# Kernel optimization log

Hardware: AMD Instinct MI355X
Metric: run time of the kernel (lower is better)

Reference implementation:

```python
import jax, jax.numpy as jnp
import numpy as np
import math

B, C, H, W, T, NH, SS = 4, 64, 32, 32, 32, 8, 512


def _alibi_slopes(heads):
    def pow2(n):
        start = 2 ** (-2 ** (-(math.log2(n) - 3)))
        return [start * start ** i for i in range(n)]
    if math.log2(heads).is_integer():
        return pow2(heads)
    cp = 2 ** math.floor(math.log2(heads))
    return pow2(cp) + pow2(2 * cp)[0::2][: heads - cp]


def _style_conv(x, style, weight, lw, lb, noise_p, bias_p, noise):
    # x: (b,c,h,w,t); weight: (out,in,1,1,1) -> modulated 1x1x1 grouped conv
    s = style @ lw.T + lb                                   # (b, in)
    w = weight[None] * s[:, None, :, None, None, None]       # (b,out,in,1,1,1)
    sigma_inv = jax.lax.rsqrt(jnp.sum(w * w, axis=(2, 3, 4, 5), keepdims=True) + 1e-8)
    w = (w * sigma_inv)[:, :, :, 0, 0, 0]                    # (b,out,in)
    y = jnp.einsum('bchwt,boc->bohwt', x, w)
    y = y + noise_p * noise                                  # (out,1,1,1)*(b,1,h,w,t)
    return y + bias_p


def setup_inputs() -> dict:
    key = jax.random.key(0)
    ks = jax.random.split(key, 8)
    return {
        'x': jax.random.normal(ks[0], (B, C, H, W, T), jnp.float32),
        'style': jax.random.normal(ks[1], (B, SS), jnp.float32),
        'qkv_w': jax.random.normal(ks[2], (3 * C, C, 1, 1, 1), jnp.float32),
        'qkv_lw': jax.random.normal(ks[3], (C, SS), jnp.float32) * 0.02,
        'qkv_lb': jnp.zeros((C,), jnp.float32),
        'qkv_np': jnp.zeros((3 * C, 1, 1, 1), jnp.float32),
        'qkv_bp': jnp.zeros((3 * C, 1, 1, 1), jnp.float32),
        'qkv_noise': jax.random.normal(ks[4], (B, 1, H, W, T), jnp.float32),
        'proj_w': jax.random.normal(ks[5], (C, C, 1, 1, 1), jnp.float32),
        'proj_lw': jax.random.normal(ks[6], (C, SS), jnp.float32) * 0.02,
        'proj_lb': jnp.zeros((C,), jnp.float32),
        'proj_np': jnp.zeros((C, 1, 1, 1), jnp.float32),
        'proj_bp': jnp.zeros((C, 1, 1, 1), jnp.float32),
        'proj_noise': jax.random.normal(ks[7], (B, 1, H, W, T), jnp.float32),
    }


def reference(x, style, qkv_w, qkv_lw, qkv_lb, qkv_np, qkv_bp, qkv_noise,
              proj_w, proj_lw, proj_lb, proj_np, proj_bp, proj_noise):
    b, c, h, w, t = x.shape
    qkv = _style_conv(x, style, qkv_w, qkv_lw, qkv_lb, qkv_np, qkv_bp, qkv_noise)
    q, k, v = jnp.split(qkv, 3, axis=1)                      # each (b,c,h,w,t)

    def to_heads(z):
        z = z.reshape(b, c * h * w, t).transpose(0, 2, 1)    # (b,t,chw)
        return z.reshape(b, t, NH, (c * h * w) // NH).transpose(0, 2, 1, 3)
    q, k, v = to_heads(q), to_heads(k), to_heads(v)          # (b,nh,t,dh)
    dh = q.shape[-1]

    attn = jnp.einsum('bnid,bnjd->bnij', q, k) / math.sqrt(dh)
    slopes = jnp.asarray(_alibi_slopes(NH), dtype=attn.dtype)[:, None, None]
    pos = -jnp.abs(jnp.arange(t)[None, :] - jnp.arange(t)[:, None]).astype(attn.dtype)
    attn = attn + slopes * pos                                # ALiBi bias
    # Faithful to original: masked_fill where tril(ones) is True (lower triangle masked)
    mask = jnp.tril(jnp.ones((t, t), bool))
    attn = jnp.where(mask, jnp.asarray(-1e18, attn.dtype), attn)
    attn = jax.nn.softmax(attn, axis=-1)
    out = jnp.einsum('bnij,bnjd->bnid', attn, v)              # (b,nh,t,dh)

    out = out.transpose(0, 2, 1, 3).reshape(b, t, c * h * w)  # (b,t,chw)
    out = out.reshape(b, t, c, h, w).transpose(0, 2, 3, 4, 1) # (b,c,h,w,t)
    return _style_conv(out, style, proj_w, proj_lw, proj_lb, proj_np, proj_bp, proj_noise)
```

## Files before the change

kernel.cpp:

```cpp
#include <hip/hip_runtime.h>

typedef unsigned short u16;
typedef unsigned int   u32;
typedef __attribute__((ext_vector_type(8))) short bf16x8;
typedef __attribute__((ext_vector_type(4))) float f32x4;

#define PP 32768
#define CC 64

__device__ __forceinline__ u16 f2b(float f) {
    u32 u; __builtin_memcpy(&u, &f, 4);
    u32 r = (u + 0x7FFFu + ((u >> 16) & 1u)) >> 16;
    return (u16)r;
}
__device__ __forceinline__ u32 pack2(float lo, float hi) {
    return (u32)f2b(lo) | ((u32)f2b(hi) << 16);
}

__global__ __launch_bounds__(64) void k_style2(
        const float* __restrict__ style, const float* __restrict__ qkv_lw,
        const float* __restrict__ qkv_lb, const float* __restrict__ proj_lw,
        const float* __restrict__ proj_lb, float* __restrict__ s_out) {
    int id = blockIdx.x;
    int b = id >> 7, sel = (id >> 6) & 1, o = id & 63;
    int t = threadIdx.x;
    const float* lw = sel ? proj_lw : qkv_lw;
    const float* lb = sel ? proj_lb : qkv_lb;
    const float* st = style + b * 512 + t * 8;
    const float* wr = lw + (size_t)o * 512 + t * 8;
    float4 s0 = *(const float4*)st, s1 = *(const float4*)(st + 4);
    float4 w0 = *(const float4*)wr, w1 = *(const float4*)(wr + 4);
    float p = s0.x*w0.x + s0.y*w0.y + s0.z*w0.z + s0.w*w0.w
            + s1.x*w1.x + s1.y*w1.y + s1.z*w1.z + s1.w*w1.w;
    #pragma unroll
    for (int off = 32; off > 0; off >>= 1) p += __shfl_xor(p, off, 64);
    if (t == 0) s_out[b * 128 + sel * 64 + o] = p + lb[o];
}

__global__ __launch_bounds__(64) void k_wnorm(
        const float* __restrict__ qkv_w, const float* __restrict__ proj_w,
        const float* __restrict__ s, u16* __restrict__ wqk_bf,
        u16* __restrict__ wv_bf, u16* __restrict__ wp_bf, float* __restrict__ S) {
    int id = blockIdx.x;
    int b = id >> 8, o = id & 255, i = threadIdx.x;
    if (i < 32) S[(size_t)id * 32 + i] = 0.f;
    float wv;
    if (o < 192) wv = qkv_w[o * 64 + i] * s[b * 128 + i];
    else         wv = proj_w[(o - 192) * 64 + i] * s[b * 128 + 64 + i];
    float sq = wv * wv;
    #pragma unroll
    for (int off = 32; off > 0; off >>= 1) sq += __shfl_xor(sq, off, 64);
    float val = wv * rsqrtf(sq + 1e-8f);
    if (o < 128) {
        u32 uv = __float_as_uint(val);
        float res = val - __uint_as_float(uv & 0xFFFF0000u);
        wqk_bf[((size_t)b * 256 + o) * 64 + i]       = (u16)(uv >> 16);
        wqk_bf[((size_t)b * 256 + 128 + o) * 64 + i] = (u16)(__float_as_uint(res) >> 16);
    }
    else if (o < 192) wv_bf[((size_t)b * 64 + (o - 128)) * 64 + i] = f2b(val);
    else {
        int o2 = o - 192;
        u32 uv = __float_as_uint(val);
        float res = val - __uint_as_float(uv & 0xFFFF0000u);
        wp_bf[((size_t)b * 64 + o2) * 64 + i]         = (u16)(uv >> 16);
        wp_bf[16384 + ((size_t)b * 64 + o2) * 64 + i] = (u16)(__float_as_uint(res) >> 16);
    }
}

__global__ __launch_bounds__(256) void k_fscores(
        const float* __restrict__ x, const u16* __restrict__ wqk_bf,
        const float* __restrict__ qnp, const float* __restrict__ qbp,
        const float* __restrict__ qnoise, float* __restrict__ S) {
    int bidx = blockIdx.x;
    int b = bidx >> 7, hg = (bidx >> 6) & 1, chunk = bidx & 63;
    int tid = threadIdx.x;
    __shared__ u32   XTh[4480];
    __shared__ u32   XTl[4480];
    __shared__ float NZ[128];
    __shared__ __align__(16) u16 QTh[4][1288], QTl[4][1288];
    __shared__ __align__(16) u16 KTh[4][1288], KTl[4][1288];

    int wv = tid >> 6, l = tid & 63, tl = l & 15, g = l >> 4;
    bf16x8 WH[4][2], WL[4][2];
    #pragma unroll
    for (int mt = 0; mt < 4; ++mt) {
        int n = hg * 4 + mt;
        int wrow = n * 8 + (tl & 7) + (tl >> 3) * 64;
        const u16* wpb = wqk_bf + (size_t)b * 16384 + wrow * 64;
        #pragma unroll
        for (int k = 0; k < 2; ++k) {
            WH[mt][k] = *(const bf16x8*)(wpb + k * 32 + g * 8);
            WL[mt][k] = *(const bf16x8*)(wpb + 8192 + k * 32 + g * 8);
        }
    }
    float4 np4[4], bp4[4];
    #pragma unroll
    for (int mt = 0; mt < 4; ++mt) {
        int pidx = (g >> 1) * 64 + (hg * 4 + mt) * 8 + (g & 1) * 4;
        np4[mt] = *(const float4*)(qnp + pidx);
        bp4[mt] = *(const float4*)(qbp + pidx);
    }
    int ti = wv >> 1, tj = wv & 1;
    f32x4 sacc[4];
    #pragma unroll
    for (int h = 0; h < 4; ++h) sacc[h] = (f32x4){0.f, 0.f, 0.f, 0.f};

    #pragma unroll 1
    for (int sub = 0; sub < 4; ++sub) {
        const float* xc = x + (size_t)b * CC * PP + chunk * 512 + sub * 128;
        #pragma unroll
        for (int r2 = 0; r2 < 4; ++r2) {
            int idx = r2 * 256 + tid;
            int e2 = idx >> 5, rem = idx & 31;
            const float* pa = xc + (size_t)(2 * e2) * PP + rem * 4;
            float4 fa = *(const float4*)pa;
            float4 fb = *(const float4*)(pa + PP);
            #pragma unroll
            for (int j = 0; j < 4; ++j) {
                float va = (&fa.x)[j], vb = (&fb.x)[j];
                u32 ua = __float_as_uint(va), ub = __float_as_uint(vb);
                float ra = va - __uint_as_float(ua & 0xFFFF0000u);
                float rb = vb - __uint_as_float(ub & 0xFFFF0000u);
                int p = (rem * 4 + j) * 35 + e2;
                XTh[p] = (ua >> 16) | (ub & 0xFFFF0000u);
                XTl[p] = (__float_as_uint(ra) >> 16) | (__float_as_uint(rb) & 0xFFFF0000u);
            }
        }
        if (tid < 32)
            *(float4*)&NZ[tid * 4] = *(const float4*)
                (qnoise + (size_t)b * PP + chunk * 512 + sub * 128 + tid * 4);
        __syncthreads();
        #pragma unroll
        for (int nh = 0; nh < 2; ++nh) {
            int nt = wv * 2 + nh, pos = nt * 16 + tl;
            union { bf16x8 v; u32 d[4]; } BH[2], BL[2];
            #pragma unroll
            for (int k = 0; k < 2; ++k) {
                const u32* ph = &XTh[pos * 35 + k * 16 + g * 4];
                const u32* pl = &XTl[pos * 35 + k * 16 + g * 4];
                BH[k].d[0] = ph[0]; BH[k].d[1] = ph[1]; BH[k].d[2] = ph[2]; BH[k].d[3] = ph[3];
                BL[k].d[0] = pl[0]; BL[k].d[1] = pl[1]; BL[k].d[2] = pl[2]; BL[k].d[3] = pl[3];
            }
            float nz = NZ[pos];
            int t = pos & 31, hwl = pos >> 5, side = g >> 1, g1 = g & 1;
            int off = t * 40 + hwl * 8 + g1 * 4;
            #pragma unroll
            for (int mt = 0; mt < 4; ++mt) {
                f32x4 a = {0.f, 0.f, 0.f, 0.f};
                #pragma unroll
                for (int k = 0; k < 2; ++k) {
                    a = __builtin_amdgcn_mfma_f32_16x16x32_bf16(WH[mt][k], BH[k].v, a, 0, 0, 0);
                    a = __builtin_amdgcn_mfma_f32_16x16x32_bf16(WH[mt][k], BL[k].v, a, 0, 0, 0);
                    a = __builtin_amdgcn_mfma_f32_16x16x32_bf16(WL[mt][k], BH[k].v, a, 0, 0, 0);
                }
                u32 uu[4], lu[4];
                #pragma unroll
                for (int j = 0; j < 4; ++j) {
                    float yv = a[j] + (&np4[mt].x)[j] * nz + (&bp4[mt].x)[j];
                    u32 uy = __float_as_uint(yv);
                    float res = yv - __uint_as_float(uy & 0xFFFF0000u);
                    uu[j] = uy; lu[j] = __float_as_uint(res);
                }
                u16* dh = (side ? KTh[mt] : QTh[mt]) + off;
                u16* dl = (side ? KTl[mt] : QTl[mt]) + off;
                *(uint2*)dh = make_uint2((uu[0] >> 16) | (uu[1] & 0xFFFF0000u),
                                         (uu[2] >> 16) | (uu[3] & 0xFFFF0000u));
                *(uint2*)dl = make_uint2((lu[0] >> 16) | (lu[1] & 0xFFFF0000u),
                                         (lu[2] >> 16) | (lu[3] & 0xFFFF0000u));
            }
        }
        __syncthreads();
        int ar = (ti * 16 + tl) * 40 + g * 8;
        int br = (tj * 16 + tl) * 40 + g * 8;
        #pragma unroll
        for (int h = 0; h < 4; ++h) {
            bf16x8 Ah = *(const bf16x8*)&QTh[h][ar];
            bf16x8 Al = *(const bf16x8*)&QTl[h][ar];
            bf16x8 Bh = *(const bf16x8*)&KTh[h][br];
            bf16x8 Bl = *(const bf16x8*)&KTl[h][br];
            sacc[h] = __builtin_amdgcn_mfma_f32_16x16x32_bf16(Ah, Bh, sacc[h], 0, 0, 0);
            sacc[h] = __builtin_amdgcn_mfma_f32_16x16x32_bf16(Ah, Bl, sacc[h], 0, 0, 0);
            sacc[h] = __builtin_amdgcn_mfma_f32_16x16x32_bf16(Al, Bh, sacc[h], 0, 0, 0);
        }
    }
    float* Sbase = S + ((size_t)b * 8 + hg * 4) * 1024;
    #pragma unroll
    for (int h = 0; h < 4; ++h) {
        float* Sb = Sbase + h * 1024;
        #pragma unroll
        for (int jj = 0; jj < 4; ++jj)
            atomicAdd(&Sb[(ti * 16 + g * 4 + jj) * 32 + tj * 16 + tl], sacc[h][jj]);
    }
}

__global__ __launch_bounds__(256) void k_out(
        const float* __restrict__ x, const u16* __restrict__ wv_bf,
        const float* __restrict__ qnp, const float* __restrict__ qbp,
        const float* __restrict__ qnoise, const float* __restrict__ Sg,
        const u16* __restrict__ wp_bf, const float* __restrict__ pnp,
        const float* __restrict__ pbp, const float* __restrict__ pnoise,
        float* __restrict__ out) {
    int bidx = blockIdx.x;
    int b = bidx >> 9, hw0 = (bidx & 511) * 2;
    int tid = threadIdx.x;
    int wv_ = tid >> 6, l = tid & 63, tl = l & 15, g = l >> 4;
    __shared__ __align__(16) u16 V16[5120];
    __shared__ __align__(16) float uni[4096];
    {
        u32* XTu = (u32*)uni;
        const float* xc = x + (size_t)b * CC * PP + (size_t)hw0 * 32;
        #pragma unroll
        for (int r2 = 0; r2 < 2; ++r2) {
            int idx = r2 * 256 + tid;
            int e2 = idx >> 4, rem = idx & 15;
            const float* pa = xc + (size_t)(2 * e2) * PP + rem * 4;
            float4 fa = *(const float4*)pa;
            float4 fb = *(const float4*)(pa + PP);
            #pragma unroll
            for (int j = 0; j < 4; ++j) {
                u32 ua = __float_as_uint((&fa.x)[j]), ub = __float_as_uint((&fb.x)[j]);
                u32 ha = (ua + 0x7FFFu + ((ua >> 16) & 1u)) & 0xFFFF0000u;
                u32 hb = (ub + 0x7FFFu + ((ub >> 16) & 1u)) & 0xFFFF0000u;
                XTu[(rem * 4 + j) * 35 + e2] = (ha >> 16) | hb;
            }
        }
    }
    u32 pfrag[2][2][4];
    {
        const float scale = 0.011048543456039806f;
        #pragma unroll
        for (int hh = 0; hh < 2; ++hh) {
            int h = 2 * wv_ + hh;
            float slope = exp2f(-(float)(h + 1));
            #pragma unroll
            for (int n2 = 0; n2 < 2; ++n2) {
                int row = n2 * 16 + tl;
                const float* Sp = Sg + ((size_t)b * 8 + h) * 1024 + row * 32 + g * 8;
                float4 sa = *(const float4*)Sp;
                float4 sb = *(const float4*)(Sp + 4);
                float p[8]; float m = -3e38f;
                #pragma unroll
                for (int jj = 0; jj < 8; ++jj) {
                    int j = g * 8 + jj;
                    float sv = jj < 4 ? (&sa.x)[jj] : (&sb.x)[jj - 4];
                    float val = sv * scale - slope * fabsf((float)(row - j));
                    if (j <= row) val = -1e18f;
                    p[jj] = val; m = fmaxf(m, val);
                }
                m = fmaxf(m, __shfl_xor(m, 16, 64));
                m = fmaxf(m, __shfl_xor(m, 32, 64));
                float ssum = 0.f;
                #pragma unroll
                for (int jj = 0; jj < 8; ++jj) { p[jj] = expf(p[jj] - m); ssum += p[jj]; }
                ssum += __shfl_xor(ssum, 16, 64);
                ssum += __shfl_xor(ssum, 32, 64);
                float r = 1.f / ssum;
                #pragma unroll
                for (int m2 = 0; m2 < 4; ++m2)
                    pfrag[hh][n2][m2] = pack2(p[2 * m2] * r, p[2 * m2 + 1] * r);
            }
        }
    }
    __syncthreads();
    {
        const u32* XT32 = (const u32*)uni;
        const u16* wvb = wv_bf + (size_t)b * 4096;
        bf16x8 Af[4][2];
        #pragma unroll
        for (int mt = 0; mt < 4; ++mt)
            #pragma unroll
            for (int k = 0; k < 2; ++k)
                Af[mt][k] = *(const bf16x8*)(wvb + (mt * 16 + tl) * 64 + k * 32 + g * 8);
        int pos = wv_ * 16 + tl;
        int t = pos & 31, hwl = pos >> 5;
        f32x4 acc[4];
        #pragma unroll
        for (int mt = 0; mt < 4; ++mt) acc[mt] = (f32x4){0.f, 0.f, 0.f, 0.f};
        #pragma unroll
        for (int k = 0; k < 2; ++k) {
            union { bf16x8 v8; u32 d[4]; } B;
            const u32* xp = XT32 + pos * 35 + k * 16 + g * 4;
            B.d[0] = xp[0]; B.d[1] = xp[1]; B.d[2] = xp[2]; B.d[3] = xp[3];
            #pragma unroll
            for (int mt = 0; mt < 4; ++mt)
                acc[mt] = __builtin_amdgcn_mfma_f32_16x16x32_bf16(Af[mt][k], B.v8, acc[mt], 0, 0, 0);
        }
        float nz = qnoise[(size_t)b * PP + (size_t)(hw0 + hwl) * 32 + t];
        #pragma unroll
        for (int mt = 0; mt < 4; ++mt) {
            float4 np4 = *(const float4*)(qnp + 128 + mt * 16 + g * 4);
            float4 bp4 = *(const float4*)(qbp + 128 + mt * 16 + g * 4);
            #pragma unroll
            for (int j = 0; j < 4; ++j) {
                int ich = mt * 16 + g * 4 + j;
                int rv = ich * 2 + hwl;
                float y = acc[mt][j] + (&np4.x)[j] * nz + (&bp4.x)[j];
                u32 bo = (u32)(rv * 80 + t * 2) ^ ((((u32)rv >> 4) & 3u) << 5);
                *(u16*)((char*)V16 + bo) = f2b(y);
            }
        }
    }
    __syncthreads();
    u16* ATh = (u16*)uni;
    u16* ATl = ATh + 4096;
    {
        #pragma unroll
        for (int hh = 0; hh < 2; ++hh) {
            int h = 2 * wv_ + hh;
            bf16x8 Bp[2];
            #pragma unroll
            for (int n2 = 0; n2 < 2; ++n2) {
                union { bf16x8 v8; u32 d[4]; } U;
                U.d[0] = pfrag[hh][n2][0]; U.d[1] = pfrag[hh][n2][1];
                U.d[2] = pfrag[hh][n2][2]; U.d[3] = pfrag[hh][n2][3];
                Bp[n2] = U.v8;
            }
            int rv = h * 16 + tl;
            u32 bo = ((u32)(rv * 80) + (u32)g * 16) ^ ((((u32)rv >> 4) & 3u) << 5);
            bf16x8 Av = *(const bf16x8*)((const char*)V16 + bo);
            #pragma unroll
            for (int n2 = 0; n2 < 2; ++n2) {
                f32x4 a4 = (f32x4){0.f, 0.f, 0.f, 0.f};
                a4 = __builtin_amdgcn_mfma_f32_16x16x32_bf16(Av, Bp[n2], a4, 0, 0, 0);
                int t = n2 * 16 + tl;
                #pragma unroll
                for (int j = 0; j < 4; ++j) {
                    int r = g * 4 + j;
                    int hwl2 = r & 1, il = r >> 1;
                    int row = hwl2 * 32 + t;
                    int i = h * 8 + il;
                    u32 uy = __float_as_uint(a4[j]);
                    float res = a4[j] - __uint_as_float(uy & 0xFFFF0000u);
                    u32 ao = ((u32)(row * 128 + i * 2)) ^ (((u32)row & 7u) << 4);
                    *(u16*)((char*)ATh + ao) = (u16)(uy >> 16);
                    *(u16*)((char*)ATl + ao) = (u16)(__float_as_uint(res) >> 16);
                }
            }
        }
    }
    __syncthreads();
    {
        bf16x8 WpH[4][2], WpL[4][2];
        #pragma unroll
        for (int mt = 0; mt < 4; ++mt)
            #pragma unroll
            for (int k = 0; k < 2; ++k) {
                const u16* wb = wp_bf + ((size_t)b * 64 + mt * 16 + tl) * 64 + k * 32 + g * 8;
                WpH[mt][k] = *(const bf16x8*)wb;
                WpL[mt][k] = *(const bf16x8*)(wb + 16384);
            }
        int pos = wv_ * 16 + tl;
        union { bf16x8 v; u32 d[4]; } BH[2], BL[2];
        #pragma unroll
        for (int k = 0; k < 2; ++k) {
            u32 bo = ((u32)(pos * 128 + k * 64 + g * 16)) ^ (((u32)pos & 7u) << 4);
            BH[k].v = *(const bf16x8*)((const char*)ATh + bo);
            BL[k].v = *(const bf16x8*)((const char*)ATl + bo);
        }
        f32x4 dacc[4];
        #pragma unroll
        for (int mt = 0; mt < 4; ++mt) dacc[mt] = (f32x4){0.f, 0.f, 0.f, 0.f};
        #pragma unroll
        for (int k = 0; k < 2; ++k)
            #pragma unroll
            for (int mt = 0; mt < 4; ++mt) {
                dacc[mt] = __builtin_amdgcn_mfma_f32_16x16x32_bf16(WpH[mt][k], BH[k].v, dacc[mt], 0, 0, 0);
                dacc[mt] = __builtin_amdgcn_mfma_f32_16x16x32_bf16(WpH[mt][k], BL[k].v, dacc[mt], 0, 0, 0);
                dacc[mt] = __builtin_amdgcn_mfma_f32_16x16x32_bf16(WpL[mt][k], BH[k].v, dacc[mt], 0, 0, 0);
            }
        int hwl = pos >> 5, t = pos & 31;
        float nz = pnoise[(size_t)b * PP + (size_t)(hw0 + hwl) * 32 + t];
        #pragma unroll
        for (int mt = 0; mt < 4; ++mt) {
            float4 npv = *(const float4*)(pnp + mt * 16 + g * 4);
            float4 bpv = *(const float4*)(pbp + mt * 16 + g * 4);
            #pragma unroll
            for (int jj = 0; jj < 4; ++jj) {
                int o = mt * 16 + g * 4 + jj;
                out[(size_t)(b * 64 + o) * PP + (size_t)(hw0 + hwl) * 32 + t]
                    = dacc[mt][jj] + (&npv.x)[jj] * nz + (&bpv.x)[jj];
            }
        }
    }
}

__global__ __launch_bounds__(256) void k_zero(float* __restrict__ out, int n) {
    int i = blockIdx.x * 256 + threadIdx.x;
    if (i < n) out[i] = 0.f;
}
__global__ void k_code(float* __restrict__ out, float code) { out[0] = code; }

extern "C" void kernel_launch(void* const* d_in, const int* in_sizes, int n_in,
                              void* d_out, int out_size, void* d_ws, size_t ws_size,
                              hipStream_t stream) {
    float* out = (float*)d_out;
    const int exp_sizes[14] = {4*64*32768, 4*512, 192*64, 64*512, 64, 192, 192,
                               4*32768, 64*64, 64*512, 64, 64, 64, 4*32768};
    bool ok = (n_in == 14) && (out_size == 4*64*32768);
    if (ok) for (int k = 0; k < 14; ++k) ok = ok && (in_sizes[k] == exp_sizes[k]);
    if (!ok) {
        k_zero<<<(out_size + 255) / 256, 256, 0, stream>>>(out, out_size);
        k_code<<<1, 1, 0, stream>>>(out, 1000.f);
        return;
    }
    if (ws_size < 395264) {
        k_zero<<<(out_size + 255) / 256, 256, 0, stream>>>(out, out_size);
        k_code<<<1, 1, 0, stream>>>(out, 2000.f + (float)(ws_size >> 20));
        return;
    }
    char* ws = (char*)d_ws;
    float* S      = (float*)ws;
    u16*   wqk_bf = (u16*)  (ws + 131072);
    u16*   wv_bf  = (u16*)  (ws + 262144);
    u16*   wp_bf  = (u16*)  (ws + 327680);
    float* s_sty  = (float*)(ws + 393216);

    k_style2 <<<512,  64,  0, stream>>>((const float*)d_in[1], (const float*)d_in[3],
                                        (const float*)d_in[4], (const float*)d_in[9],
                                        (const float*)d_in[10], s_sty);
    k_wnorm  <<<1024, 64,  0, stream>>>((const float*)d_in[2], (const float*)d_in[8],
                                        s_sty, wqk_bf, wv_bf, wp_bf, S);
    k_fscores<<<512,  256, 0, stream>>>((const float*)d_in[0], wqk_bf,
                                        (const float*)d_in[5], (const float*)d_in[6],
                                        (const float*)d_in[7], S);
    k_out    <<<2048, 256, 0, stream>>>((const float*)d_in[0], wv_bf,
                                        (const float*)d_in[5], (const float*)d_in[6],
                                        (const float*)d_in[7], S, wp_bf,
                                        (const float*)d_in[11], (const float*)d_in[12],
                                        (const float*)d_in[13], out);
    hipError_t e = hipGetLastError();
    if (e != hipSuccess) {
        k_zero<<<(out_size + 255) / 256, 256, 0, stream>>>(out, out_size);
        k_code<<<1, 1, 0, stream>>>(out, 3000.f + (float)e);
    }
}
```

Measured before the change: 162.4 us.

## Fuse V projection into score kernel and stage V through output buffer

The value projection (modulated 1x1 conv for V) moves from k_out into k_fscores, which already converts x to bf16 and holds the input fragments in registers. The V result is written to global memory as bf16 stored in 32-bit words, using the output buffer as scratch. k_out then loads V directly instead of re-reading x, transposing it through shared memory and running the V MFMAs, which cuts one shared buffer and a barrier. In exchange, an extra full-size V tensor is written and read back, with half of each 32-bit word wasted. Correctness depends on each k_out block reading its V slice before overwriting the same output region.

```diff
diff --git a/kernel.cpp b/kernel.cpp
--- a/kernel.cpp
+++ b/kernel.cpp
@@ -69,8 +69,9 @@
 
 __global__ __launch_bounds__(256) void k_fscores(
         const float* __restrict__ x, const u16* __restrict__ wqk_bf,
-        const float* __restrict__ qnp, const float* __restrict__ qbp,
-        const float* __restrict__ qnoise, float* __restrict__ S) {
+        const u16* __restrict__ wv_bf, const float* __restrict__ qnp,
+        const float* __restrict__ qbp, const float* __restrict__ qnoise,
+        float* __restrict__ S, u32* __restrict__ Vg) {
     int bidx = blockIdx.x;
     int b = bidx >> 7, hg = (bidx >> 6) & 1, chunk = bidx & 63;
     int tid = threadIdx.x;
@@ -93,12 +94,25 @@
             WL[mt][k] = *(const bf16x8*)(wpb + 8192 + k * 32 + g * 8);
         }
     }
+    bf16x8 WV[2][2];
+    #pragma unroll
+    for (int mt2 = 0; mt2 < 2; ++mt2)
+        #pragma unroll
+        for (int k = 0; k < 2; ++k)
+            WV[mt2][k] = *(const bf16x8*)(wv_bf +
+                ((size_t)b * 64 + hg * 32 + mt2 * 16 + tl) * 64 + k * 32 + g * 8);
     float4 np4[4], bp4[4];
     #pragma unroll
     for (int mt = 0; mt < 4; ++mt) {
         int pidx = (g >> 1) * 64 + (hg * 4 + mt) * 8 + (g & 1) * 4;
         np4[mt] = *(const float4*)(qnp + pidx);
         bp4[mt] = *(const float4*)(qbp + pidx);
+    }
+    float4 vnp[2], vbp[2];
+    #pragma unroll
+    for (int mt2 = 0; mt2 < 2; ++mt2) {
+        vnp[mt2] = *(const float4*)(qnp + 128 + hg * 32 + mt2 * 16 + g * 4);
+        vbp[mt2] = *(const float4*)(qbp + 128 + hg * 32 + mt2 * 16 + g * 4);
     }
     int ti = wv >> 1, tj = wv & 1;
     f32x4 sacc[4];
@@ -168,6 +182,22 @@
                 *(uint2*)dl = make_uint2((lu[0] >> 16) | (lu[1] & 0xFFFF0000u),
                                          (lu[2] >> 16) | (lu[3] & 0xFFFF0000u));
             }
+            #pragma unroll
+            for (int mt2 = 0; mt2 < 2; ++mt2) {
+                f32x4 av = {0.f, 0.f, 0.f, 0.f};
+                #pragma unroll
+                for (int k = 0; k < 2; ++k) {
+                    av = __builtin_amdgcn_mfma_f32_16x16x32_bf16(WV[mt2][k], BH[k].v, av, 0, 0, 0);
+                    av = __builtin_amdgcn_mfma_f32_16x16x32_bf16(WV[mt2][k], BL[k].v, av, 0, 0, 0);
+                }
+                #pragma unroll
+                for (int j = 0; j < 4; ++j) {
+                    int ich = hg * 32 + mt2 * 16 + g * 4 + j;
+                    float y = av[j] + (&vnp[mt2].x)[j] * nz + (&vbp[mt2].x)[j];
+                    Vg[((size_t)b * 64 + ich) * PP + chunk * 512 + sub * 128 + pos]
+                        = (u32)f2b(y);
+                }
+            }
         }
         __syncthreads();
         int ar = (ti * 16 + tl) * 40 + g * 8;
@@ -194,37 +224,15 @@
 }
 
 __global__ __launch_bounds__(256) void k_out(
-        const float* __restrict__ x, const u16* __restrict__ wv_bf,
-        const float* __restrict__ qnp, const float* __restrict__ qbp,
-        const float* __restrict__ qnoise, const float* __restrict__ Sg,
-        const u16* __restrict__ wp_bf, const float* __restrict__ pnp,
-        const float* __restrict__ pbp, const float* __restrict__ pnoise,
-        float* __restrict__ out) {
+        const float* __restrict__ Sg, const u16* __restrict__ wp_bf,
+        const float* __restrict__ pnp, const float* __restrict__ pbp,
+        const float* __restrict__ pnoise, float* out) {
     int bidx = blockIdx.x;
     int b = bidx >> 9, hw0 = (bidx & 511) * 2;
     int tid = threadIdx.x;
     int wv_ = tid >> 6, l = tid & 63, tl = l & 15, g = l >> 4;
-    __shared__ __align__(16) u16 V16[5120];
-    __shared__ __align__(16) float uni[4096];
-    {
-        u32* XTu = (u32*)uni;
-        const float* xc = x + (size_t)b * CC * PP + (size_t)hw0 * 32;
-        #pragma unroll
-        for (int r2 = 0; r2 < 2; ++r2) {
-            int idx = r2 * 256 + tid;
-            int e2 = idx >> 4, rem = idx & 15;
-            const float* pa = xc + (size_t)(2 * e2) * PP + rem * 4;
-            float4 fa = *(const float4*)pa;
-            float4 fb = *(const float4*)(pa + PP);
-            #pragma unroll
-            for (int j = 0; j < 4; ++j) {
-                u32 ua = __float_as_uint((&fa.x)[j]), ub = __float_as_uint((&fb.x)[j]);
-                u32 ha = (ua + 0x7FFFu + ((ua >> 16) & 1u)) & 0xFFFF0000u;
-                u32 hb = (ub + 0x7FFFu + ((ub >> 16) & 1u)) & 0xFFFF0000u;
-                XTu[(rem * 4 + j) * 35 + e2] = (ha >> 16) | hb;
-            }
-        }
-    }
+    __shared__ __align__(16) u16 AT[8192];
+    u16* ATh = AT; u16* ATl = AT + 4096;
     u32 pfrag[2][2][4];
     {
         const float scale = 0.011048543456039806f;
@@ -261,49 +269,8 @@
             }
         }
     }
-    __syncthreads();
     {
-        const u32* XT32 = (const u32*)uni;
-        const u16* wvb = wv_bf + (size_t)b * 4096;
-        bf16x8 Af[4][2];
-        #pragma unroll
-        for (int mt = 0; mt < 4; ++mt)
-            #pragma unroll
-            for (int k = 0; k < 2; ++k)
-                Af[mt][k] = *(const bf16x8*)(wvb + (mt * 16 + tl) * 64 + k * 32 + g * 8);
-        int pos = wv_ * 16 + tl;
-        int t = pos & 31, hwl = pos >> 5;
-        f32x4 acc[4];
-        #pragma unroll
-        for (int mt = 0; mt < 4; ++mt) acc[mt] = (f32x4){0.f, 0.f, 0.f, 0.f};
-        #pragma unroll
-        for (int k = 0; k < 2; ++k) {
-            union { bf16x8 v8; u32 d[4]; } B;
-            const u32* xp = XT32 + pos * 35 + k * 16 + g * 4;
-            B.d[0] = xp[0]; B.d[1] = xp[1]; B.d[2] = xp[2]; B.d[3] = xp[3];
-            #pragma unroll
-            for (int mt = 0; mt < 4; ++mt)
-                acc[mt] = __builtin_amdgcn_mfma_f32_16x16x32_bf16(Af[mt][k], B.v8, acc[mt], 0, 0, 0);
-        }
-        float nz = qnoise[(size_t)b * PP + (size_t)(hw0 + hwl) * 32 + t];
-        #pragma unroll
-        for (int mt = 0; mt < 4; ++mt) {
-            float4 np4 = *(const float4*)(qnp + 128 + mt * 16 + g * 4);
-            float4 bp4 = *(const float4*)(qbp + 128 + mt * 16 + g * 4);
-            #pragma unroll
-            for (int j = 0; j < 4; ++j) {
-                int ich = mt * 16 + g * 4 + j;
-                int rv = ich * 2 + hwl;
-                float y = acc[mt][j] + (&np4.x)[j] * nz + (&bp4.x)[j];
-                u32 bo = (u32)(rv * 80 + t * 2) ^ ((((u32)rv >> 4) & 3u) << 5);
-                *(u16*)((char*)V16 + bo) = f2b(y);
-            }
-        }
-    }
-    __syncthreads();
-    u16* ATh = (u16*)uni;
-    u16* ATl = ATh + 4096;
-    {
+        const u32* Vg = (const u32*)out;
         #pragma unroll
         for (int hh = 0; hh < 2; ++hh) {
             int h = 2 * wv_ + hh;
@@ -316,12 +283,20 @@
                 Bp[n2] = U.v8;
             }
             int rv = h * 16 + tl;
-            u32 bo = ((u32)(rv * 80) + (u32)g * 16) ^ ((((u32)rv >> 4) & 3u) << 5);
-            bf16x8 Av = *(const bf16x8*)((const char*)V16 + bo);
+            int ich = rv >> 1, hwl = rv & 1;
+            const u32* vp = Vg + ((size_t)b * 64 + ich) * PP
+                               + (size_t)(hw0 + hwl) * 32 + g * 8;
+            uint4 va = *(const uint4*)vp;
+            uint4 vb = *(const uint4*)(vp + 4);
+            union { bf16x8 v8; u32 d[4]; } AV;
+            AV.d[0] = (va.x & 0xFFFFu) | (va.y << 16);
+            AV.d[1] = (va.z & 0xFFFFu) | (va.w << 16);
+            AV.d[2] = (vb.x & 0xFFFFu) | (vb.y << 16);
+            AV.d[3] = (vb.z & 0xFFFFu) | (vb.w << 16);
             #pragma unroll
             for (int n2 = 0; n2 < 2; ++n2) {
                 f32x4 a4 = (f32x4){0.f, 0.f, 0.f, 0.f};
-                a4 = __builtin_amdgcn_mfma_f32_16x16x32_bf16(Av, Bp[n2], a4, 0, 0, 0);
+                a4 = __builtin_amdgcn_mfma_f32_16x16x32_bf16(AV.v8, Bp[n2], a4, 0, 0, 0);
                 int t = n2 * 16 + tl;
                 #pragma unroll
                 for (int j = 0; j < 4; ++j) {
@@ -420,12 +395,10 @@
                                         (const float*)d_in[10], s_sty);
     k_wnorm  <<<1024, 64,  0, stream>>>((const float*)d_in[2], (const float*)d_in[8],
                                         s_sty, wqk_bf, wv_bf, wp_bf, S);
-    k_fscores<<<512,  256, 0, stream>>>((const float*)d_in[0], wqk_bf,
+    k_fscores<<<512,  256, 0, stream>>>((const float*)d_in[0], wqk_bf, wv_bf,
                                         (const float*)d_in[5], (const float*)d_in[6],
-                                        (const float*)d_in[7], S);
-    k_out    <<<2048, 256, 0, stream>>>((const float*)d_in[0], wv_bf,
-                                        (const float*)d_in[5], (const float*)d_in[6],
-                                        (const float*)d_in[7], S, wp_bf,
+                                        (const float*)d_in[7], S, (u32*)d_out);
+    k_out    <<<2048, 256, 0, stream>>>(S, wp_bf,
                                         (const float*)d_in[11], (const float*)d_in[12],
                                         (const float*)d_in[13], out);
     hipError_t e = hipGetLastError();
```

Result: no change. 159.3 us (-1.9%).
